# Optimization experiments

Hardware: AMD Instinct MI355X
Metric: run time of the kernel (lower is better)

Reference implementation:

```python
import jax, jax.numpy as jnp
import numpy as np

IN_DIM = 1024
OUT_DIM = 1024
NUM_HEADS = 16
DEPTH = IN_DIM // NUM_HEADS  # 64


def setup_inputs() -> dict:
    key = jax.random.key(0)
    ks = jax.random.split(key, 11)
    B, S = 8, 1024  # S must equal IN_DIM (reshape constraint in original module)
    s_in = 1.0 / np.sqrt(IN_DIM)
    return {
        "query": jax.random.normal(ks[0], (B, S, IN_DIM), jnp.float32),
        "key": jax.random.normal(ks[1], (B, S, IN_DIM), jnp.float32),
        "value": jax.random.normal(ks[2], (B, S, IN_DIM), jnp.float32),
        "Wq": jax.random.normal(ks[3], (IN_DIM, IN_DIM), jnp.float32) * s_in,
        "bq": jnp.zeros((IN_DIM,), jnp.float32),
        "Wk": jax.random.normal(ks[4], (IN_DIM, IN_DIM), jnp.float32) * s_in,
        "bk": jnp.zeros((IN_DIM,), jnp.float32),
        "Wv": jax.random.normal(ks[5], (IN_DIM, IN_DIM), jnp.float32) * s_in,
        "bv": jnp.zeros((IN_DIM,), jnp.float32),
        "Wo": jax.random.normal(ks[6], (OUT_DIM, IN_DIM), jnp.float32) * s_in,
        "bo": jnp.zeros((OUT_DIM,), jnp.float32),
    }


def reference(query, key, value, Wq, bq, Wk, bk, Wv, bv, Wo, bo):
    B, S, D = query.shape
    H, P = NUM_HEADS, DEPTH

    def split_heads(x):
        # (B,S,D) -> (B,S,H,P) -> transpose last two dims -> (B,S,P,H)
        return x.reshape(B, S, H, P).swapaxes(-1, -2)

    Q = split_heads(query @ Wq.T + bq)   # (B,S,P,H)
    K = split_heads(key @ Wk.T + bk)     # (B,S,P,H)
    V = split_heads(value @ Wv.T + bv)   # (B,S,P,H)

    scale = jnp.sqrt(jnp.float32(P))
    # scores over the depth axis, per (batch, token): (B,S,P,P)
    scores = jnp.einsum('bsph,bsqh->bspq', Q, K) / scale
    # original uses softmax over dim=0 (the batch axis) - reproduce faithfully
    attn = jax.nn.softmax(scores, axis=0)
    out = jnp.einsum('bspq,bsqh->bsph', attn, V)   # (B,S,P,H)
    # transpose(-1,-2) -> (B,S,H,P), reshape to (B,S,S) (requires H*P == S)
    out = out.swapaxes(-1, -2).reshape(B, S, S)
    out = out @ Wo.T + bo                           # (B,S,OUT_DIM)
    return jax.nn.sigmoid(out)
```

## Files before the change

### kernel.cpp

```cpp
#include <hip/hip_runtime.h>


using short8   = __attribute__((ext_vector_type(8))) short;
using floatx4  = __attribute__((ext_vector_type(4))) float;
using floatx16 = __attribute__((ext_vector_type(16))) float;

__device__ __forceinline__ float bf2f(unsigned short u) {
    return __uint_as_float(((unsigned)u) << 16);
}
__device__ __forceinline__ unsigned short f2bf(float f) {
    unsigned u = __float_as_uint(f);
    u += 0x7fffu + ((u >> 16) & 1u);
    return (unsigned short)(u >> 16);
}
__device__ __forceinline__ unsigned pack_trunc(float f0, float f1) {
    return __builtin_amdgcn_perm(__float_as_uint(f1), __float_as_uint(f0), 0x07060302u);
}
__device__ __forceinline__ void async_ld16(const void* g, void* l) {
    __builtin_amdgcn_global_load_lds(
        (const __attribute__((address_space(1))) unsigned int*)g,
        (__attribute__((address_space(3))) unsigned int*)l, 16, 0, 0);
}

__device__ __forceinline__ void conv8(const float* src, unsigned short* d, size_t i) {
    float4 a = *(const float4*)(src + i);
    float4 b = *(const float4*)(src + i + 4);
    uint4 o;
    o.x = ((unsigned)f2bf(a.y) << 16) | f2bf(a.x);
    o.y = ((unsigned)f2bf(a.w) << 16) | f2bf(a.z);
    o.z = ((unsigned)f2bf(b.y) << 16) | f2bf(b.x);
    o.w = ((unsigned)f2bf(b.w) << 16) | f2bf(b.z);
    *(uint4*)(d + i) = o;
}

__global__ __launch_bounds__(256) void convert_weights(
    const float* __restrict__ w0, const float* __restrict__ w1,
    const float* __restrict__ w2, const float* __restrict__ w3,
    unsigned short* __restrict__ dst)
{
    const float* srcs[4] = {w0, w1, w2, w3};
    conv8(srcs[blockIdx.y], dst + (size_t)blockIdx.y * (1024u * 1024u),
          ((size_t)blockIdx.x * 256 + threadIdx.x) * 8);
}

__global__ __launch_bounds__(256) void convert_acts(
    const float* __restrict__ a0, const float* __restrict__ a1,
    const float* __restrict__ a2, unsigned short* __restrict__ dst)
{
    const float* srcs[3] = {a0, a1, a2};
    conv8(srcs[blockIdx.y], dst + (size_t)blockIdx.y * ((size_t)8192 * 1024),
          ((size_t)blockIdx.x * 256 + threadIdx.x) * 8);
}

template<bool AF32, bool SIG>
__global__ __launch_bounds__(256) void gemm128(
    const void* __restrict__ A0, const void* __restrict__ A1, const void* __restrict__ A2,
    const unsigned short* __restrict__ W0, const unsigned short* __restrict__ W1,
    const unsigned short* __restrict__ W2,
    const float* __restrict__ b0, const float* __restrict__ b1, const float* __restrict__ b2,
    void* __restrict__ C0, void* __restrict__ C1, void* __restrict__ C2)
{
    const int z = blockIdx.z;
    const void* Ap = (z == 0) ? A0 : (z == 1) ? A1 : A2;
    const unsigned short* W = (z == 0) ? W0 : (z == 1) ? W1 : W2;
    const float* bias = (z == 0) ? b0 : (z == 1) ? b1 : b2;
    void* Cp = (z == 0) ? C0 : (z == 1) ? C1 : C2;

    constexpr int Kd = 1024, Nd = 1024;
    const int t = threadIdx.x;
    const int w = t >> 6, lane = t & 63;
    const int l15 = lane & 15, quad = lane >> 4;
    const int blockM = blockIdx.x * 128;
    const int blockN = blockIdx.y * 128;
    const int wy = w >> 1, wx = w & 1;

    __shared__ unsigned short Bs[128 * 32];
    constexpr int ABYTES = AF32 ? (128 * 32 * 4) : (128 * 32 * 2);
    __shared__ __align__(16) unsigned char AsRaw[ABYTES];
    float* AsF = (float*)AsRaw;
    unsigned short* AsB = (unsigned short*)AsRaw;

    const int br  = lane >> 2;
    const int bg  = (lane & 3) ^ (br & 3);
    const unsigned short* Bsrc0 = W + (size_t)(blockN + w * 32 + br) * Kd + bg * 8;
    const unsigned short* Bsrc1 = Bsrc0 + (size_t)16 * Kd;
    unsigned short* Bdst0 = &Bs[(w * 2 + 0) * 512];
    unsigned short* Bdst1 = &Bs[(w * 2 + 1) * 512];

    const int ar = lane >> 3;
    const int ag = (lane & 7) ^ (ar & 7);
    const float* AsrcF[4];
    float* AdstF[4];
    const unsigned short* AsrcB0 = nullptr; const unsigned short* AsrcB1 = nullptr;
    unsigned short* AdstB0 = nullptr; unsigned short* AdstB1 = nullptr;
    if (AF32) {
        #pragma unroll
        for (int j = 0; j < 4; ++j) {
            AsrcF[j] = (const float*)Ap + (size_t)(blockM + w * 32 + j * 8 + ar) * Kd + ag * 4;
            AdstF[j] = AsF + (w * 4 + j) * 256;
        }
    } else {
        AsrcB0 = (const unsigned short*)Ap + (size_t)(blockM + w * 32 + br) * Kd + bg * 8;
        AsrcB1 = AsrcB0 + (size_t)16 * Kd;
        AdstB0 = &AsB[(w * 2 + 0) * 512];
        AdstB1 = &AsB[(w * 2 + 1) * 512];
    }

    floatx4 acc[4][4] = {};

    for (int k0 = 0; k0 < Kd; k0 += 32) {
        if (AF32) {
            #pragma unroll
            for (int j = 0; j < 4; ++j) async_ld16(AsrcF[j] + k0, AdstF[j]);
        } else {
            async_ld16(AsrcB0 + k0, AdstB0);
            async_ld16(AsrcB1 + k0, AdstB1);
        }
        async_ld16(Bsrc0 + k0, Bdst0);
        async_ld16(Bsrc1 + k0, Bdst1);
        __syncthreads();

        short8 af[4], bfr[4];
        #pragma unroll
        for (int mt = 0; mt < 4; ++mt) {
            const int row = wy * 64 + mt * 16 + l15;
            if (AF32) {
                const int r7 = l15 & 7;
                const float* ap = AsF + row * 32;
                float4 lo = *(const float4*)(ap + (((quad * 2 + 0) ^ r7) * 4));
                float4 hi = *(const float4*)(ap + (((quad * 2 + 1) ^ r7) * 4));
                union { unsigned u[4]; short8 s; } cv;
                cv.u[0] = pack_trunc(lo.x, lo.y);
                cv.u[1] = pack_trunc(lo.z, lo.w);
                cv.u[2] = pack_trunc(hi.x, hi.y);
                cv.u[3] = pack_trunc(hi.z, hi.w);
                af[mt] = cv.s;
            } else {
                af[mt] = *(const short8*)&AsB[row * 32 + (quad ^ (l15 & 3)) * 8];
            }
        }
        #pragma unroll
        for (int nt = 0; nt < 4; ++nt) {
            const int row = wx * 64 + nt * 16 + l15;
            bfr[nt] = *(const short8*)&Bs[row * 32 + (quad ^ (l15 & 3)) * 8];
        }
        #pragma unroll
        for (int mt = 0; mt < 4; ++mt)
            #pragma unroll
            for (int nt = 0; nt < 4; ++nt)
                acc[mt][nt] = __builtin_amdgcn_mfma_f32_16x16x32_bf16(af[mt], bfr[nt], acc[mt][nt], 0, 0, 0);
        __syncthreads();
    }

    #pragma unroll
    for (int nt = 0; nt < 4; ++nt) {
        const int col = blockN + wx * 64 + nt * 16 + l15;
        const float bv = bias[col];
        #pragma unroll
        for (int mt = 0; mt < 4; ++mt) {
            const int row = blockM + wy * 64 + mt * 16 + quad * 4;
            #pragma unroll
            for (int r = 0; r < 4; ++r) {
                float v = acc[mt][nt][r] + bv;
                if (SIG) {
                    v = 1.0f / (1.0f + __expf(-v));
                    ((float*)Cp)[(size_t)(row + r) * Nd + col] = v;
                } else {
                    ((unsigned short*)Cp)[(size_t)(row + r) * Nd + col] = f2bf(v);
                }
            }
        }
    }
}

__global__ __launch_bounds__(512) void attn_mfma(
    const unsigned short* __restrict__ Q,
    const unsigned short* __restrict__ Kt,
    const unsigned short* __restrict__ Vt,
    unsigned short* __restrict__ O2)
{
    constexpr int VOFF = 0;
    constexpr int UOFF = 9216;
    constexpr int QOFF = UOFF + 8192;
    __shared__ __align__(16) unsigned short lds[UOFF + 18432];

    const int s  = blockIdx.x;
    const int ph = blockIdx.y;
    const int t  = threadIdx.x;
    const int w  = t >> 6;
    const int l  = t & 63;
    const int l15 = l & 15, l31 = l & 31, half = l >> 5, quad = l >> 4;

    const size_t gb = ((size_t)w * 1024 + s) * 1024;

    {
        const unsigned* vg = (const unsigned*)(Vt + gb);
        unsigned* vd = (unsigned*)lds;
        #pragma unroll
        for (int it = 0; it < 8; ++it) {
            const int h = it * 2 + half;
            vd[w * 576 + h * 36 + l31] = vg[h * 32 + l31];
        }
        const unsigned short* kg = Kt + gb;
        unsigned* kd = (unsigned*)(lds + UOFF);
        #pragma unroll
        for (int h2 = 0; h2 < 8; ++h2) {
            unsigned klo = kg[(2 * h2) * 64 + l];
            unsigned khi = kg[(2 * h2 + 1) * 64 + l];
            kd[w * 512 + l * 8 + h2] = klo | (khi << 16);
        }
        const unsigned short* qg = Q + gb + ph * 32;
        unsigned* qd = (unsigned*)(lds + QOFF);
        #pragma unroll
        for (int it = 0; it < 4; ++it) {
            const int h = it * 4 + half * 2;
            unsigned qlo = qg[h * 64 + l31];
            unsigned qhi = qg[(h + 1) * 64 + l31];
            qd[w * 256 + l31 * 8 + it * 2 + half] = qlo | (qhi << 16);
        }
    }
    __syncthreads();

    floatx16 sc[2];
    {
        short8 qf = *(const short8*)&lds[QOFF + w * 512 + l31 * 16 + half * 8];
        short8 kf0 = *(const short8*)&lds[UOFF + w * 1024 + l31 * 16 + half * 8];
        short8 kf1 = *(const short8*)&lds[UOFF + w * 1024 + (32 + l31) * 16 + half * 8];
        floatx16 z = {};
        sc[0] = __builtin_amdgcn_mfma_f32_32x32x16_bf16(kf0, qf, z, 0, 0, 0);
        sc[1] = __builtin_amdgcn_mfma_f32_32x32x16_bf16(kf1, qf, z, 0, 0, 0);
    }
    __syncthreads();

    {
        unsigned short* sx = lds + UOFF + w * 2304 + l31 * 72;
        #pragma unroll
        for (int nt = 0; nt < 2; ++nt) {
            #pragma unroll
            for (int rg = 0; rg < 4; ++rg) {
                float e0 = __expf(sc[nt][4 * rg + 0] * 0.125f);
                float e1 = __expf(sc[nt][4 * rg + 1] * 0.125f);
                float e2 = __expf(sc[nt][4 * rg + 2] * 0.125f);
                float e3 = __expf(sc[nt][4 * rg + 3] * 0.125f);
                uint2 pk = { pack_trunc(e0, e1), pack_trunc(e2, e3) };
                const int q0 = nt * 32 + rg * 8 + half * 4;
                *(uint2*)&sx[q0] = pk;
            }
        }
    }
    __syncthreads();

    {
        const int p  = t & 31;
        const int q0 = (t >> 5) * 4;
        unsigned short* base = lds + UOFF + p * 72 + q0;
        float fv[8][4];
        float den0 = 0.f, den1 = 0.f, den2 = 0.f, den3 = 0.f;
        #pragma unroll
        for (int b = 0; b < 8; ++b) {
            uint2 v = *(const uint2*)&base[b * 2304];
            fv[b][0] = bf2f((unsigned short)(v.x & 0xffff));
            fv[b][1] = bf2f((unsigned short)(v.x >> 16));
            fv[b][2] = bf2f((unsigned short)(v.y & 0xffff));
            fv[b][3] = bf2f((unsigned short)(v.y >> 16));
            den0 += fv[b][0]; den1 += fv[b][1]; den2 += fv[b][2]; den3 += fv[b][3];
        }
        const float r0 = __builtin_amdgcn_rcpf(den0);
        const float r1 = __builtin_amdgcn_rcpf(den1);
        const float r2 = __builtin_amdgcn_rcpf(den2);
        const float r3 = __builtin_amdgcn_rcpf(den3);
        #pragma unroll
        for (int b = 0; b < 8; ++b) {
            uint2 pk = { pack_trunc(fv[b][0] * r0, fv[b][1] * r1),
                         pack_trunc(fv[b][2] * r2, fv[b][3] * r3) };
            *(uint2*)&base[b * 2304] = pk;
        }
    }
    __syncthreads();

    floatx4 o[2] = {};
    #pragma unroll
    for (int qc = 0; qc < 2; ++qc) {
        short8 vf = *(const short8*)&lds[VOFF + w * 1152 + l15 * 72 + qc * 32 + quad * 8];
        #pragma unroll
        for (int mt = 0; mt < 2; ++mt) {
            short8 wf = *(const short8*)&lds[UOFF + w * 2304 + (mt * 16 + l15) * 72 + qc * 32 + quad * 8];
            o[mt] = __builtin_amdgcn_mfma_f32_16x16x32_bf16(wf, vf, o[mt], 0, 0, 0);
        }
    }
    {
        unsigned short* ol = lds + UOFF + w * 2304 + l15 * 36;
        #pragma unroll
        for (int mt = 0; mt < 2; ++mt) {
            uint2 pk = { pack_trunc(o[mt][0], o[mt][1]), pack_trunc(o[mt][2], o[mt][3]) };
            *(uint2*)&ol[mt * 16 + quad * 4] = pk;
        }
    }
    __syncthreads();

    {
        unsigned* outdw = (unsigned*)O2;
        const unsigned* ol = (const unsigned*)(lds + UOFF + w * 2304);
        const size_t gdw = ((size_t)w * 1024 + s) * 512 + ph * 16;
        #pragma unroll
        for (int i = 0; i < 4; ++i) {
            const int d = i * 64 + l;
            const int h = d >> 4, pq = d & 15;
            outdw[gdw + h * 32 + pq] = ol[h * 18 + pq];
        }
    }
}

extern "C" void kernel_launch(void* const* d_in, const int* in_sizes, int n_in,
                              void* d_out, int out_size, void* d_ws, size_t ws_size,
                              hipStream_t stream) {
    const float* query = (const float*)d_in[0];
    const float* key_  = (const float*)d_in[1];
    const float* value = (const float*)d_in[2];
    const float* Wq = (const float*)d_in[3];
    const float* bq = (const float*)d_in[4];
    const float* Wk = (const float*)d_in[5];
    const float* bk = (const float*)d_in[6];
    const float* Wv = (const float*)d_in[7];
    const float* bv = (const float*)d_in[8];
    const float* Wo = (const float*)d_in[9];
    const float* bo = (const float*)d_in[10];

    const size_t WN = (size_t)1024 * 1024;
    const size_t MN = (size_t)8192 * 1024;

    unsigned short* Wbf = (unsigned short*)d_ws;
    unsigned short* Wq_bf = Wbf;
    unsigned short* Wk_bf = Wbf + WN;
    unsigned short* Wv_bf = Wbf + 2 * WN;
    unsigned short* Wo_bf = Wbf + 3 * WN;

    convert_weights<<<dim3(512, 4), dim3(256), 0, stream>>>(Wq, Wk, Wv, Wo, Wbf);

    const bool big = ws_size >= (4 * WN + 6 * MN) * sizeof(unsigned short);

    unsigned short* Qb; unsigned short* Kb; unsigned short* Vb;
    if (big) {
        unsigned short* abf = Wbf + 4 * WN;
        Qb = abf + 3 * MN; Kb = Qb + MN; Vb = Kb + MN;
        convert_acts<<<dim3(4096, 3), dim3(256), 0, stream>>>(query, key_, value, abf);
        gemm128<false, false><<<dim3(64, 8, 3), dim3(256), 0, stream>>>(
            abf, abf + MN, abf + 2 * MN, Wq_bf, Wk_bf, Wv_bf, bq, bk, bv, Qb, Kb, Vb);
    } else {
        Qb = Wbf + 4 * WN; Kb = Qb + MN; Vb = Kb + MN;
        gemm128<true, false><<<dim3(64, 8, 3), dim3(256), 0, stream>>>(
            query, key_, value, Wq_bf, Wk_bf, Wv_bf, bq, bk, bv, Qb, Kb, Vb);
    }

    unsigned short* O2 = Qb;
    attn_mfma<<<dim3(1024, 2), dim3(512), 0, stream>>>(Qb, Kb, Vb, O2);

    gemm128<false, true><<<dim3(64, 8, 1), dim3(256), 0, stream>>>(
        O2, O2, O2, Wo_bf, Wo_bf, Wo_bf, bo, bo, bo, d_out, d_out, d_out);
}
```

Measured before the change: 280.3 us.

## Replace 128-tile GEMMs with 256x256 tile, 4-stage async-LDS pipelined MFMA GEMM

Adds a gemm256 kernel with 512 threads, 256x256 output tiles, 32x32x16 bf16 MFMA and a 4-stage ring of global-to-LDS async loads with swizzled layout and explicit vmcnt waits. It is used for both the QKV projection and the output projection with sigmoid. Larger tiles raise data reuse per global load, and the deeper pipeline is meant to hide memory latency. In exchange, about 128KB of LDS per block limits each CU to one block. The grids of 384 and 128 blocks may leave CUs idle or create a tail wave.

```diff
diff --git a/kernel.cpp b/kernel.cpp
--- a/kernel.cpp
+++ b/kernel.cpp
@@ -173,6 +173,150 @@
     }
 }
 
+#define VM8 do { asm volatile("s_waitcnt vmcnt(8)" ::: "memory"); \
+                 __builtin_amdgcn_sched_barrier(0); } while (0)
+#define VM4 do { asm volatile("s_waitcnt vmcnt(4)" ::: "memory"); \
+                 __builtin_amdgcn_sched_barrier(0); } while (0)
+#define VM0 do { asm volatile("s_waitcnt vmcnt(0)" ::: "memory"); \
+                 __builtin_amdgcn_sched_barrier(0); } while (0)
+#define BARRIER __builtin_amdgcn_s_barrier()
+
+#define STAGE_T(s, k0) do { \
+    async_ld16(srcA[0] + (k0), &lds[s][0][dA0]); \
+    async_ld16(srcA[1] + (k0), &lds[s][0][dA1]); \
+    async_ld16(srcB[0] + (k0), &lds[s][1][dA0]); \
+    async_ld16(srcB[1] + (k0), &lds[s][1][dA1]); \
+} while (0)
+
+#define PHASE_T(s, STG, VMW) do { \
+    short8 afr[4][2], bfr2[2][2]; \
+    const unsigned short* As_ = lds[s][0]; \
+    const unsigned short* Bs_ = lds[s][1]; \
+    _Pragma("unroll") \
+    for (int mf = 0; mf < 4; ++mf) \
+      _Pragma("unroll") \
+      for (int ks = 0; ks < 2; ++ks) \
+        afr[mf][ks] = *(const short8*)&As_[aoff[mf][ks]]; \
+    _Pragma("unroll") \
+    for (int nf = 0; nf < 2; ++nf) \
+      _Pragma("unroll") \
+      for (int ks = 0; ks < 2; ++ks) \
+        bfr2[nf][ks] = *(const short8*)&Bs_[boff[nf][ks]]; \
+    STG; \
+    VMW; \
+    BARRIER; \
+    __builtin_amdgcn_s_setprio(1); \
+    _Pragma("unroll") \
+    for (int ks = 0; ks < 2; ++ks) \
+      _Pragma("unroll") \
+      for (int mf = 0; mf < 4; ++mf) \
+        _Pragma("unroll") \
+        for (int nf = 0; nf < 2; ++nf) \
+          acc[mf][nf] = __builtin_amdgcn_mfma_f32_32x32x16_bf16( \
+              afr[mf][ks], bfr2[nf][ks], acc[mf][nf], 0, 0, 0); \
+    __builtin_amdgcn_s_setprio(0); \
+    BARRIER; \
+} while (0)
+
+template<bool SIG>
+__global__ __launch_bounds__(512, 2) void gemm256(
+    const unsigned short* __restrict__ A0, const unsigned short* __restrict__ A1,
+    const unsigned short* __restrict__ A2,
+    const unsigned short* __restrict__ W0, const unsigned short* __restrict__ W1,
+    const unsigned short* __restrict__ W2,
+    const float* __restrict__ b0, const float* __restrict__ b1, const float* __restrict__ b2,
+    void* __restrict__ C0, void* __restrict__ C1, void* __restrict__ C2)
+{
+    const int z = blockIdx.z;
+    const unsigned short* A = (z == 0) ? A0 : (z == 1) ? A1 : A2;
+    const unsigned short* W = (z == 0) ? W0 : (z == 1) ? W1 : W2;
+    const float* bias = (z == 0) ? b0 : (z == 1) ? b1 : b2;
+    void* Cp = (z == 0) ? C0 : (z == 1) ? C1 : C2;
+
+    constexpr int Kd = 1024;
+    const int t = threadIdx.x;
+    const int w = t >> 6, l = t & 63;
+    const int wy = w >> 2, wx = w & 3;
+    const int l31 = l & 31, h5 = l >> 5;
+    const int blockM = blockIdx.x * 256;
+    const int blockN = blockIdx.y * 256;
+
+    __shared__ __align__(16) unsigned short lds[4][2][8192];
+
+    const unsigned short* srcA[2];
+    const unsigned short* srcB[2];
+    #pragma unroll
+    for (int i = 0; i < 2; ++i) {
+        const int q  = i * 512 + w * 64 + l;
+        const int L  = q >> 3;
+        const int Gr = (q & 7) ^ (L & 7);
+        const int r  = L * 2 + (Gr >> 2);
+        const int g  = Gr & 3;
+        srcA[i] = A + (size_t)(blockM + r) * Kd + g * 8;
+        srcB[i] = W + (size_t)(blockN + r) * Kd + g * 8;
+    }
+    const int dA0 = (0 * 512 + w * 64) * 8;
+    const int dA1 = (1 * 512 + w * 64) * 8;
+
+    const int Lh  = l31 >> 1;
+    const int la7 = Lh & 7;
+    const int e4  = (l & 1) * 4;
+    int aoff[4][2], boff[2][2];
+    #pragma unroll
+    for (int mf = 0; mf < 4; ++mf)
+        #pragma unroll
+        for (int ks = 0; ks < 2; ++ks)
+            aoff[mf][ks] = (wy * 64 + mf * 16 + Lh) * 64 + ((e4 + ks * 2 + h5) ^ la7) * 8;
+    #pragma unroll
+    for (int nf = 0; nf < 2; ++nf)
+        #pragma unroll
+        for (int ks = 0; ks < 2; ++ks)
+            boff[nf][ks] = (wx * 32 + nf * 16 + Lh) * 64 + ((e4 + ks * 2 + h5) ^ la7) * 8;
+
+    floatx16 acc[4][2] = {};
+
+    STAGE_T(0, 0); STAGE_T(1, 32); STAGE_T(2, 64);
+    VM8;
+    BARRIER;
+
+    int k0 = 96;
+    #pragma unroll 1
+    for (int tt = 0; tt < 28; tt += 4) {
+        PHASE_T(0, STAGE_T(3, k0), VM8); k0 += 32;
+        PHASE_T(1, STAGE_T(0, k0), VM8); k0 += 32;
+        PHASE_T(2, STAGE_T(1, k0), VM8); k0 += 32;
+        PHASE_T(3, STAGE_T(2, k0), VM8); k0 += 32;
+    }
+    PHASE_T(0, STAGE_T(3, k0), VM8);
+    PHASE_T(1, (void)0, VM4);
+    PHASE_T(2, (void)0, VM0);
+    PHASE_T(3, (void)0, (void)0);
+
+    const int colBase = blockN + wx * 64 + l31;
+    const float bv0 = bias[colBase];
+    const float bv1 = bias[colBase + 32];
+    #pragma unroll
+    for (int mf = 0; mf < 4; ++mf) {
+        const int row0 = blockM + wy * 128 + mf * 32 + h5 * 4;
+        #pragma unroll
+        for (int nf = 0; nf < 2; ++nf) {
+            const float bb = nf ? bv1 : bv0;
+            const int col = colBase + nf * 32;
+            #pragma unroll
+            for (int rg = 0; rg < 16; ++rg) {
+                const int row = row0 + (rg & 3) + 8 * (rg >> 2);
+                float v = acc[mf][nf][rg] + bb;
+                if (SIG) {
+                    v = 1.0f / (1.0f + __expf(-v));
+                    ((float*)Cp)[(size_t)row * 1024 + col] = v;
+                } else {
+                    ((unsigned short*)Cp)[(size_t)row * 1024 + col] = f2bf(v);
+                }
+            }
+        }
+    }
+}
+
 __global__ __launch_bounds__(512) void attn_mfma(
     const unsigned short* __restrict__ Q,
     const unsigned short* __restrict__ Kt,
@@ -344,7 +488,7 @@
         unsigned short* abf = Wbf + 4 * WN;
         Qb = abf + 3 * MN; Kb = Qb + MN; Vb = Kb + MN;
         convert_acts<<<dim3(4096, 3), dim3(256), 0, stream>>>(query, key_, value, abf);
-        gemm128<false, false><<<dim3(64, 8, 3), dim3(256), 0, stream>>>(
+        gemm256<false><<<dim3(32, 4, 3), dim3(512), 0, stream>>>(
             abf, abf + MN, abf + 2 * MN, Wq_bf, Wk_bf, Wv_bf, bq, bk, bv, Qb, Kb, Vb);
     } else {
         Qb = Wbf + 4 * WN; Kb = Qb + MN; Vb = Kb + MN;
@@ -355,6 +499,6 @@
     unsigned short* O2 = Qb;
     attn_mfma<<<dim3(1024, 2), dim3(512), 0, stream>>>(Qb, Kb, Vb, O2);
 
-    gemm128<false, true><<<dim3(64, 8, 1), dim3(256), 0, stream>>>(
+    gemm256<true><<<dim3(32, 4, 1), dim3(512), 0, stream>>>(
         O2, O2, O2, Wo_bf, Wo_bf, Wo_bf, bo, bo, bo, d_out, d_out, d_out);
 }
```

Result: slower. 291.6 us (+4.0%).
